# Performance work log

Measured on AMD Instinct MI355X. Metric: run time of the kernel, lower is better.

Reference implementation:

```python
import jax, jax.numpy as jnp
import numpy as np

MARGIN = 1.0  # init kwarg
BIG = 1e9     # finite sentinel for masked reductions (dist in [0, 2])


def setup_inputs() -> dict:
    key = jax.random.key(0)
    k1, k2 = jax.random.split(key)
    embeddings = jax.random.normal(k1, (8192, 256), dtype=jnp.float32)
    labels = jax.random.randint(k2, (8192,), 0, 128)
    return {"embeddings": embeddings, "labels": labels}


def reference(embeddings, labels):
    # cosine distance matrix: 1 - x_hat @ x_hat^T, clamped at 0
    norm = jnp.linalg.norm(embeddings, axis=1, keepdims=True)
    x = embeddings / jnp.maximum(norm, 1e-12)  # matches F.normalize eps
    dist = jnp.clip(1.0 - x @ x.T, 0.0, None)  # (B, B)

    same = labels[:, None] == labels[None, :]
    eye = jnp.eye(labels.shape[0], dtype=bool)
    pos_mask = same & ~eye   # same label, different index
    neg_mask = ~same         # different label

    # hard mining: hardest positive (max dist), hardest negative (min dist)
    pos_dist = jnp.max(jnp.where(pos_mask, dist, -BIG), axis=1)  # (B,)
    neg_dist = jnp.min(jnp.where(neg_mask, dist, BIG), axis=1)   # (B,)

    valid = pos_mask.any(axis=1) & neg_mask.any(axis=1)          # (B,)
    per_anchor = jnp.maximum(pos_dist - neg_dist + MARGIN, 0.0)
    loss_sum = jnp.sum(jnp.where(valid, per_anchor, 0.0))
    count = jnp.sum(valid).astype(dist.dtype)
    return jnp.where(count > 0, loss_sum / jnp.maximum(count, 1.0), 0.0)
```

## Files before the change

### kernel.cpp

```cpp
#include <hip/hip_runtime.h>
#include <hip/hip_bf16.h>


constexpr int NB = 8192;
constexpr int ND = 256;
constexpr int TI = 128;
constexpr int BJ = 64;
constexpr int NT = NB / TI;
constexpr int NPAIR = NT * (NT + 1) / 2;
constexpr int NITER = TI / BJ;

typedef __attribute__((ext_vector_type(8))) short bf16x8;
typedef __attribute__((ext_vector_type(4))) float f32x4;

typedef __attribute__((address_space(3))) unsigned int lds_u32;
typedef __attribute__((address_space(1))) const unsigned int g_u32;

__device__ inline void load_lds16(const unsigned short* g, unsigned short* l) {
    __builtin_amdgcn_global_load_lds((g_u32*)g, (lds_u32*)l, 16, 0, 0);
}

__device__ inline unsigned short f2bf(float v) {
    __hip_bfloat16 b = __float2bfloat16(v);
    return *reinterpret_cast<unsigned short*>(&b);
}

__global__ __launch_bounds__(256) void norm_kernel(const float* __restrict__ X,
                                                   unsigned short* __restrict__ Xbt,
                                                   float* accum, int* done) {
    const int t = threadIdx.x;
    const int rb = blockIdx.x * 32;
    const int r = t >> 3, e = t & 7;
    if (blockIdx.x == 0 && t == 0) { accum[0] = 0.f; accum[1] = 0.f; *done = 0; }

    const float4* src = (const float4*)(X + (size_t)(rb + r) * ND + e * 32);
    float4 v[8];
    #pragma unroll
    for (int k = 0; k < 8; k++) v[k] = src[k];

    float s = 0.f;
    #pragma unroll
    for (int k = 0; k < 8; k++) {
        s += v[k].x * v[k].x; s += v[k].y * v[k].y;
        s += v[k].z * v[k].z; s += v[k].w * v[k].w;
    }
    #pragma unroll
    for (int m = 1; m <= 4; m <<= 1) s += __shfl_xor(s, m, 64);
    const float sc = 1.0f / fmaxf(sqrtf(s), 1e-12f);

    #pragma unroll
    for (int k = 0; k < 4; k++) {
        const float* f = (const float*)&v[2 * k];
        unsigned short tmp[8];
        #pragma unroll
        for (int q = 0; q < 8; q++) tmp[q] = f2bf(f[q] * sc);
        *(bf16x8*)(Xbt + ((size_t)(e * 4 + k) * NB + rb + r) * 8) = *(bf16x8*)tmp;
    }
}

__global__ __launch_bounds__(256, 3) void mine_kernel(
    const unsigned short* __restrict__ Xbt, const int* __restrict__ labels,
    float* __restrict__ posP, float* __restrict__ negP) {
    __shared__ __align__(16) unsigned short Bt[32 * 512];
    __shared__ int Lall[TI];
    __shared__ float colMn[4][BJ], colMx[4][BJ];

    const int tid = threadIdx.x;
    const int w = tid >> 6;
    const int lane = tid & 63;
    const int quad = lane >> 4;
    const int l16 = lane & 15;

    int ti = 0, rem = blockIdx.x;
    while (rem >= NT - ti) { rem -= NT - ti; ti++; }
    const int tj = ti + rem;

    const int rowbase = ti * TI + w * 32;
    const int jstart = tj * TI;

    if (tid < TI) Lall[tid] = labels[jstart + tid];

    bf16x8 afrag[2][8];
    #pragma unroll
    for (int rs = 0; rs < 2; rs++)
        #pragma unroll
        for (int kc = 0; kc < 8; kc++) {
            const size_t u = (size_t)(kc * 4 + quad) * NB + (rowbase + rs * 16 + l16);
            afrag[rs][kc] = *(const bf16x8*)(Xbt + u * 8);
        }

    unsigned int lpack[2];
    #pragma unroll
    for (int rs = 0; rs < 2; rs++) {
        unsigned int p = 0;
        #pragma unroll
        for (int r = 0; r < 4; r++)
            p |= ((unsigned int)labels[rowbase + rs * 16 + quad * 4 + r] & 0xffu)
                 << (8 * r);
        lpack[rs] = p;
    }

    float minK[2][4], maxK[2][4];
    #pragma unroll
    for (int rs = 0; rs < 2; rs++)
        #pragma unroll
        for (int r = 0; r < 4; r++) { minK[rs][r] = 1e30f; maxK[rs][r] = -1e30f; }

    auto stage = [&](int jt) {
        const int jbase = jstart + jt * BJ;
        #pragma unroll
        for (int s = 0; s < 8; s++) {
            const int rg = w * 8 + s;
            const int kc = rg >> 2, nfi = rg & 3;
            const size_t u = (size_t)(kc * 4 + quad) * NB + (jbase + nfi * 16 + l16);
            load_lds16(Xbt + u * 8, Bt + rg * 512);
        }
    };

    stage(0);
    __syncthreads();

    #pragma unroll 1
    for (int jt = 0; jt < NITER; jt++) {
        #pragma unroll
        for (int nf = 0; nf < 4; nf++) {
            const int flc = Lall[jt * BJ + nf * 16 + l16];
            f32x4 acc[2];
            #pragma unroll
            for (int rs = 0; rs < 2; rs++) acc[rs] = (f32x4){0.f, 0.f, 0.f, 0.f};
            #pragma unroll
            for (int kc = 0; kc < 8; kc++) {
                const bf16x8 b = *(const bf16x8*)(Bt + (kc * 4 + nf) * 512 + lane * 8);
                #pragma unroll
                for (int rs = 0; rs < 2; rs++)
                    acc[rs] = __builtin_amdgcn_mfma_f32_16x16x32_bf16(
                        afrag[rs][kc], b, acc[rs], 0, 0, 0);
            }
            float cP = 1e30f, cN = -1e30f;
            #pragma unroll
            for (int rs = 0; rs < 2; rs++)
                #pragma unroll
                for (int r = 0; r < 4; r++) {
                    const int lr = (int)((lpack[rs] >> (8 * r)) & 0xffu);
                    const float key = acc[rs][r] + ((lr != flc) ? 8.0f : 0.0f);
                    minK[rs][r] = fminf(minK[rs][r], key);
                    maxK[rs][r] = fmaxf(maxK[rs][r], key);
                    cP = fminf(cP, key);
                    cN = fmaxf(cN, key);
                }
            cP = fminf(cP, __shfl_xor(cP, 16, 64));
            cP = fminf(cP, __shfl_xor(cP, 32, 64));
            cN = fmaxf(cN, __shfl_xor(cN, 16, 64));
            cN = fmaxf(cN, __shfl_xor(cN, 32, 64));
            if (quad == 0) {
                colMn[w][nf * 16 + l16] = cP;
                colMx[w][nf * 16 + l16] = cN;
            }
        }
        __syncthreads();
        if (jt + 1 < NITER) stage(jt + 1);
        if (tid < BJ) {
            float m = colMn[0][tid];
            #pragma unroll
            for (int ww = 1; ww < 4; ww++) m = fminf(m, colMn[ww][tid]);
            posP[(size_t)ti * NB + jstart + jt * BJ + tid] = m;
        } else if (tid < 2 * BJ) {
            const int c = tid - BJ;
            float M = colMx[0][c];
            #pragma unroll
            for (int ww = 1; ww < 4; ww++) M = fmaxf(M, colMx[ww][c]);
            negP[(size_t)ti * NB + jstart + jt * BJ + c] = M;
        }
        __syncthreads();
    }

    #pragma unroll
    for (int rs = 0; rs < 2; rs++)
        #pragma unroll
        for (int r = 0; r < 4; r++) {
            float p = minK[rs][r], n = maxK[rs][r];
            #pragma unroll
            for (int m = 1; m <= 8; m <<= 1) {
                p = fminf(p, __shfl_xor(p, m, 64));
                n = fmaxf(n, __shfl_xor(n, m, 64));
            }
            if (l16 == 0) {
                const int row = rowbase + rs * 16 + quad * 4 + r;
                posP[(size_t)tj * NB + row] = p;
                negP[(size_t)tj * NB + row] = n;
            }
        }
}

__global__ __launch_bounds__(256) void finish_kernel(
    const float* __restrict__ posP, const float* __restrict__ negP,
    float* accum, int* done, float* __restrict__ out) {
    const int i = blockIdx.x * 256 + threadIdx.x;
    float p = 1e30f, n = -1e30f;
    for (int u = 0; u < NT; u++) {
        p = fminf(p, posP[(size_t)u * NB + i]);
        n = fmaxf(n, negP[(size_t)u * NB + i]);
    }
    const bool valid = (p < 4.0f) && (n > 4.0f);
    const float pos_d = fmaxf(1.0f - p, 0.0f);
    const float neg_d = fmaxf(1.0f - (n - 8.0f), 0.0f);
    float per = valid ? fmaxf(pos_d - neg_d + 1.0f, 0.0f) : 0.0f;
    float cnt = valid ? 1.0f : 0.0f;
    #pragma unroll
    for (int off = 32; off > 0; off >>= 1) {
        per += __shfl_down(per, off, 64);
        cnt += __shfl_down(cnt, off, 64);
    }
    __shared__ float sp[4], sc[4];
    const int wv = threadIdx.x >> 6, ln = threadIdx.x & 63;
    if (ln == 0) { sp[wv] = per; sc[wv] = cnt; }
    __syncthreads();
    if (threadIdx.x == 0) {
        atomicAdd(&accum[0], sp[0] + sp[1] + sp[2] + sp[3]);
        atomicAdd(&accum[1], sc[0] + sc[1] + sc[2] + sc[3]);
        __threadfence();
        const int old = atomicAdd(done, 1);
        if (old == (int)gridDim.x - 1) {
            const float s = __hip_atomic_load(&accum[0], __ATOMIC_RELAXED,
                                              __HIP_MEMORY_SCOPE_AGENT);
            const float c = __hip_atomic_load(&accum[1], __ATOMIC_RELAXED,
                                              __HIP_MEMORY_SCOPE_AGENT);
            out[0] = (c > 0.f) ? s / fmaxf(c, 1.f) : 0.f;
        }
    }
}

extern "C" void kernel_launch(void* const* d_in, const int* in_sizes, int n_in,
                              void* d_out, int out_size, void* d_ws, size_t ws_size,
                              hipStream_t stream) {
    const float* X = (const float*)d_in[0];
    const int* labels = (const int*)d_in[1];
    float* out = (float*)d_out;

    char* ws = (char*)d_ws;
    unsigned short* Xbt = (unsigned short*)ws;
    float* posP = (float*)(ws + (size_t)4 * 1024 * 1024);
    float* negP = posP + (size_t)NT * NB;
    float* accum = negP + (size_t)NT * NB;
    int* done = (int*)(accum + 2);

    norm_kernel<<<NB / 32, 256, 0, stream>>>(X, Xbt, accum, done);
    mine_kernel<<<NPAIR, 256, 0, stream>>>(
        (const unsigned short*)Xbt, labels, posP, negP);
    finish_kernel<<<NB / 256, 256, 0, stream>>>(posP, negP, accum, done, out);
}
```

Baseline: 100.4 us.

## Switch mining GEMM from 16x16x32 to 32x32x16 bf16 MFMA tiles

Replaces the 16x16x32 MFMA with the 32x32x16 variant. Each wave now computes a 32x32 output block per column chunk, and the A-fragment layout, B staging layout, label packing and the row/column reduction shuffles are all rewritten to match the new accumulator layout. The larger tile is meant to cut LDS fragment reads and instruction count per output. The trade-off is a 16-register accumulator plus 16 min/max registers per lane, which raises register pressure at the occupancy target of 3 blocks.

```diff
diff --git a/kernel.cpp b/kernel.cpp
--- a/kernel.cpp
+++ b/kernel.cpp
@@ -11,7 +11,7 @@
 constexpr int NITER = TI / BJ;
 
 typedef __attribute__((ext_vector_type(8))) short bf16x8;
-typedef __attribute__((ext_vector_type(4))) float f32x4;
+typedef __attribute__((ext_vector_type(16))) float f32x16;
 
 typedef __attribute__((address_space(3))) unsigned int lds_u32;
 typedef __attribute__((address_space(1))) const unsigned int g_u32;
@@ -68,8 +68,8 @@
     const int tid = threadIdx.x;
     const int w = tid >> 6;
     const int lane = tid & 63;
-    const int quad = lane >> 4;
-    const int l16 = lane & 15;
+    const int hi = lane >> 5;
+    const int l32 = lane & 31;
 
     int ti = 0, rem = blockIdx.x;
     while (rem >= NT - ti) { rem -= NT - ti; ti++; }
@@ -80,39 +80,35 @@
 
     if (tid < TI) Lall[tid] = labels[jstart + tid];
 
-    bf16x8 afrag[2][8];
-    #pragma unroll
-    for (int rs = 0; rs < 2; rs++)
-        #pragma unroll
-        for (int kc = 0; kc < 8; kc++) {
-            const size_t u = (size_t)(kc * 4 + quad) * NB + (rowbase + rs * 16 + l16);
-            afrag[rs][kc] = *(const bf16x8*)(Xbt + u * 8);
-        }
-
-    unsigned int lpack[2];
-    #pragma unroll
-    for (int rs = 0; rs < 2; rs++) {
+    bf16x8 afrag[16];
+    #pragma unroll
+    for (int ks = 0; ks < 16; ks++) {
+        const size_t u = (size_t)(2 * ks + hi) * NB + (rowbase + l32);
+        afrag[ks] = *(const bf16x8*)(Xbt + u * 8);
+    }
+
+    unsigned int lpack[4];
+    #pragma unroll
+    for (int g = 0; g < 4; g++) {
         unsigned int p = 0;
         #pragma unroll
-        for (int r = 0; r < 4; r++)
-            p |= ((unsigned int)labels[rowbase + rs * 16 + quad * 4 + r] & 0xffu)
-                 << (8 * r);
-        lpack[rs] = p;
-    }
-
-    float minK[2][4], maxK[2][4];
-    #pragma unroll
-    for (int rs = 0; rs < 2; rs++)
-        #pragma unroll
-        for (int r = 0; r < 4; r++) { minK[rs][r] = 1e30f; maxK[rs][r] = -1e30f; }
+        for (int b = 0; b < 4; b++)
+            p |= ((unsigned int)labels[rowbase + b + 8 * g + 4 * hi] & 0xffu)
+                 << (8 * b);
+        lpack[g] = p;
+    }
+
+    float minK[16], maxK[16];
+    #pragma unroll
+    for (int r = 0; r < 16; r++) { minK[r] = 1e30f; maxK[r] = -1e30f; }
 
     auto stage = [&](int jt) {
         const int jbase = jstart + jt * BJ;
         #pragma unroll
         for (int s = 0; s < 8; s++) {
             const int rg = w * 8 + s;
-            const int kc = rg >> 2, nfi = rg & 3;
-            const size_t u = (size_t)(kc * 4 + quad) * NB + (jbase + nfi * 16 + l16);
+            const size_t u = (size_t)(2 * (rg >> 1) + hi) * NB
+                             + (jbase + (rg & 1) * 32 + l32);
             load_lds16(Xbt + u * 8, Bt + rg * 512);
         }
     };
@@ -123,38 +119,30 @@
     #pragma unroll 1
     for (int jt = 0; jt < NITER; jt++) {
         #pragma unroll
-        for (int nf = 0; nf < 4; nf++) {
-            const int flc = Lall[jt * BJ + nf * 16 + l16];
-            f32x4 acc[2];
-            #pragma unroll
-            for (int rs = 0; rs < 2; rs++) acc[rs] = (f32x4){0.f, 0.f, 0.f, 0.f};
-            #pragma unroll
-            for (int kc = 0; kc < 8; kc++) {
-                const bf16x8 b = *(const bf16x8*)(Bt + (kc * 4 + nf) * 512 + lane * 8);
-                #pragma unroll
-                for (int rs = 0; rs < 2; rs++)
-                    acc[rs] = __builtin_amdgcn_mfma_f32_16x16x32_bf16(
-                        afrag[rs][kc], b, acc[rs], 0, 0, 0);
+        for (int cb = 0; cb < 2; cb++) {
+            const int flc = Lall[jt * BJ + cb * 32 + l32];
+            f32x16 acc = {};
+            #pragma unroll
+            for (int ks = 0; ks < 16; ks++) {
+                const bf16x8 b = *(const bf16x8*)(Bt + (ks * 2 + cb) * 512 + lane * 8);
+                acc = __builtin_amdgcn_mfma_f32_32x32x16_bf16(afrag[ks], b, acc,
+                                                              0, 0, 0);
             }
             float cP = 1e30f, cN = -1e30f;
             #pragma unroll
-            for (int rs = 0; rs < 2; rs++)
-                #pragma unroll
-                for (int r = 0; r < 4; r++) {
-                    const int lr = (int)((lpack[rs] >> (8 * r)) & 0xffu);
-                    const float key = acc[rs][r] + ((lr != flc) ? 8.0f : 0.0f);
-                    minK[rs][r] = fminf(minK[rs][r], key);
-                    maxK[rs][r] = fmaxf(maxK[rs][r], key);
-                    cP = fminf(cP, key);
-                    cN = fmaxf(cN, key);
-                }
-            cP = fminf(cP, __shfl_xor(cP, 16, 64));
+            for (int reg = 0; reg < 16; reg++) {
+                const int lr = (int)((lpack[reg >> 2] >> (8 * (reg & 3))) & 0xffu);
+                const float key = acc[reg] + ((lr != flc) ? 8.0f : 0.0f);
+                minK[reg] = fminf(minK[reg], key);
+                maxK[reg] = fmaxf(maxK[reg], key);
+                cP = fminf(cP, key);
+                cN = fmaxf(cN, key);
+            }
             cP = fminf(cP, __shfl_xor(cP, 32, 64));
-            cN = fmaxf(cN, __shfl_xor(cN, 16, 64));
             cN = fmaxf(cN, __shfl_xor(cN, 32, 64));
-            if (quad == 0) {
-                colMn[w][nf * 16 + l16] = cP;
-                colMx[w][nf * 16 + l16] = cN;
+            if (hi == 0) {
+                colMn[w][cb * 32 + l32] = cP;
+                colMx[w][cb * 32 + l32] = cN;
             }
         }
         __syncthreads();
@@ -175,21 +163,19 @@
     }
 
     #pragma unroll
-    for (int rs = 0; rs < 2; rs++)
-        #pragma unroll
-        for (int r = 0; r < 4; r++) {
-            float p = minK[rs][r], n = maxK[rs][r];
-            #pragma unroll
-            for (int m = 1; m <= 8; m <<= 1) {
-                p = fminf(p, __shfl_xor(p, m, 64));
-                n = fmaxf(n, __shfl_xor(n, m, 64));
-            }
-            if (l16 == 0) {
-                const int row = rowbase + rs * 16 + quad * 4 + r;
-                posP[(size_t)tj * NB + row] = p;
-                negP[(size_t)tj * NB + row] = n;
-            }
-        }
+    for (int reg = 0; reg < 16; reg++) {
+        float p = minK[reg], n = maxK[reg];
+        #pragma unroll
+        for (int m = 1; m <= 16; m <<= 1) {
+            p = fminf(p, __shfl_xor(p, m, 64));
+            n = fmaxf(n, __shfl_xor(n, m, 64));
+        }
+        if (l32 == 0) {
+            const int row = rowbase + (reg & 3) + 8 * (reg >> 2) + 4 * hi;
+            posP[(size_t)tj * NB + row] = p;
+            negP[(size_t)tj * NB + row] = n;
+        }
+    }
 }
 
 __global__ __launch_bounds__(256) void finish_kernel(
```

Result: slower. 115.2 us (+14.8%).

## Process a strip of up to four column tiles per mining block

Applied to the files above, without the earlier changes.

Each mining block now handles a strip of up to four consecutive upper-triangular column tiles for one row tile, instead of a single tile pair. This reuses the A-fragment register loads and labels across more column work and cuts the block count from 2080 to 544. Row-side reductions are written to per-strip slots (64+strip) rather than per-tile slots, and the finish kernel reads only the valid partial slots for its row tile. The trade-off is fewer, longer blocks, which may load-balance worse across CUs.

```diff
diff --git a/kernel.cpp b/kernel.cpp
--- a/kernel.cpp
+++ b/kernel.cpp
@@ -7,8 +7,9 @@
 constexpr int TI = 128;
 constexpr int BJ = 64;
 constexpr int NT = NB / TI;
-constexpr int NPAIR = NT * (NT + 1) / 2;
-constexpr int NITER = TI / BJ;
+constexpr int SW = 4;
+constexpr int NBLK = 544;
+constexpr int NSLOT = 80;
 
 typedef __attribute__((ext_vector_type(8))) short bf16x8;
 typedef __attribute__((ext_vector_type(4))) float f32x4;
@@ -62,7 +63,7 @@
     const unsigned short* __restrict__ Xbt, const int* __restrict__ labels,
     float* __restrict__ posP, float* __restrict__ negP) {
     __shared__ __align__(16) unsigned short Bt[32 * 512];
-    __shared__ int Lall[TI];
+    __shared__ int Lall[SW * TI];
     __shared__ float colMn[4][BJ], colMx[4][BJ];
 
     const int tid = threadIdx.x;
@@ -72,13 +73,17 @@
     const int l16 = lane & 15;
 
     int ti = 0, rem = blockIdx.x;
-    while (rem >= NT - ti) { rem -= NT - ti; ti++; }
-    const int tj = ti + rem;
+    int ns = (NT - ti + SW - 1) >> 2;
+    while (rem >= ns) { rem -= ns; ti++; ns = (NT - ti + SW - 1) >> 2; }
+    const int st = rem;
+    const int tjs = ti + st * SW;
+    const int WT = min(SW, NT - tjs);
+    const int NJ = 2 * WT;
 
     const int rowbase = ti * TI + w * 32;
-    const int jstart = tj * TI;
-
-    if (tid < TI) Lall[tid] = labels[jstart + tid];
+    const int cstart = tjs * TI;
+
+    for (int x = tid; x < WT * TI; x += 256) Lall[x] = labels[cstart + x];
 
     bf16x8 afrag[2][8];
     #pragma unroll
@@ -106,11 +111,11 @@
         #pragma unroll
         for (int r = 0; r < 4; r++) { minK[rs][r] = 1e30f; maxK[rs][r] = -1e30f; }
 
-    auto stage = [&](int jt) {
-        const int jbase = jstart + jt * BJ;
-        #pragma unroll
-        for (int s = 0; s < 8; s++) {
-            const int rg = w * 8 + s;
+    auto stage = [&](int jj) {
+        const int jbase = cstart + jj * BJ;
+        #pragma unroll
+        for (int s_ = 0; s_ < 8; s_++) {
+            const int rg = w * 8 + s_;
             const int kc = rg >> 2, nfi = rg & 3;
             const size_t u = (size_t)(kc * 4 + quad) * NB + (jbase + nfi * 16 + l16);
             load_lds16(Xbt + u * 8, Bt + rg * 512);
@@ -121,10 +126,10 @@
     __syncthreads();
 
     #pragma unroll 1
-    for (int jt = 0; jt < NITER; jt++) {
+    for (int jj = 0; jj < NJ; jj++) {
         #pragma unroll
         for (int nf = 0; nf < 4; nf++) {
-            const int flc = Lall[jt * BJ + nf * 16 + l16];
+            const int flc = Lall[jj * BJ + nf * 16 + l16];
             f32x4 acc[2];
             #pragma unroll
             for (int rs = 0; rs < 2; rs++) acc[rs] = (f32x4){0.f, 0.f, 0.f, 0.f};
@@ -158,18 +163,18 @@
             }
         }
         __syncthreads();
-        if (jt + 1 < NITER) stage(jt + 1);
+        if (jj + 1 < NJ) stage(jj + 1);
         if (tid < BJ) {
             float m = colMn[0][tid];
             #pragma unroll
             for (int ww = 1; ww < 4; ww++) m = fminf(m, colMn[ww][tid]);
-            posP[(size_t)ti * NB + jstart + jt * BJ + tid] = m;
+            posP[(size_t)ti * NB + cstart + jj * BJ + tid] = m;
         } else if (tid < 2 * BJ) {
             const int c = tid - BJ;
             float M = colMx[0][c];
             #pragma unroll
             for (int ww = 1; ww < 4; ww++) M = fmaxf(M, colMx[ww][c]);
-            negP[(size_t)ti * NB + jstart + jt * BJ + c] = M;
+            negP[(size_t)ti * NB + cstart + jj * BJ + c] = M;
         }
         __syncthreads();
     }
@@ -186,8 +191,8 @@
             }
             if (l16 == 0) {
                 const int row = rowbase + rs * 16 + quad * 4 + r;
-                posP[(size_t)tj * NB + row] = p;
-                negP[(size_t)tj * NB + row] = n;
+                posP[(size_t)(64 + st) * NB + row] = p;
+                negP[(size_t)(64 + st) * NB + row] = n;
             }
         }
 }
@@ -196,10 +201,16 @@
     const float* __restrict__ posP, const float* __restrict__ negP,
     float* accum, int* done, float* __restrict__ out) {
     const int i = blockIdx.x * 256 + threadIdx.x;
+    const int t = i >> 7;
     float p = 1e30f, n = -1e30f;
-    for (int u = 0; u < NT; u++) {
+    for (int u = 0; u <= t; u++) {
         p = fminf(p, posP[(size_t)u * NB + i]);
         n = fmaxf(n, negP[(size_t)u * NB + i]);
+    }
+    const int nst = (NT - t + SW - 1) >> 2;
+    for (int s2 = 0; s2 < nst; s2++) {
+        p = fminf(p, posP[(size_t)(64 + s2) * NB + i]);
+        n = fmaxf(n, negP[(size_t)(64 + s2) * NB + i]);
     }
     const bool valid = (p < 4.0f) && (n > 4.0f);
     const float pos_d = fmaxf(1.0f - p, 0.0f);
@@ -240,12 +251,12 @@
     char* ws = (char*)d_ws;
     unsigned short* Xbt = (unsigned short*)ws;
     float* posP = (float*)(ws + (size_t)4 * 1024 * 1024);
-    float* negP = posP + (size_t)NT * NB;
-    float* accum = negP + (size_t)NT * NB;
+    float* negP = posP + (size_t)NSLOT * NB;
+    float* accum = negP + (size_t)NSLOT * NB;
     int* done = (int*)(accum + 2);
 
     norm_kernel<<<NB / 32, 256, 0, stream>>>(X, Xbt, accum, done);
-    mine_kernel<<<NPAIR, 256, 0, stream>>>(
+    mine_kernel<<<NBLK, 256, 0, stream>>>(
         (const unsigned short*)Xbt, labels, posP, negP);
     finish_kernel<<<NB / 256, 256, 0, stream>>>(posP, negP, accum, done, out);
 }
```

After: 114.4 us. 1.14x slower.
